# Performance work log

Hardware: AMD Instinct MI355X
Metric: run time of the kernel (lower is better)

## Reference

```python
import math
import jax, jax.numpy as jnp
import numpy as np

# h_data constants (init_kwargs)
PITCH = 0.0003      # [m]
FS = 40000000.0     # [Hz]
TX_ANGLE = 0.1      # [rad]
C = 1540.0          # [m/s]
T0 = 0.0            # [s]
CLIP = -70.0        # [dB]
EPS = np.float32(np.finfo(np.float32).eps)


def interplin(v, ds, sq):
    """Vectorized per-column linear interpolation: v(sq[:,k], k).
    v: (N, K) float, sq: (N, K) query points in physical units, ds: step size.
    """
    n = v.shape[0]
    iq = sq / ds
    oob = ~(iq < n - 2)
    iqc = jnp.where(oob, 0.0, iq)
    fl = jnp.floor(iqc).astype(jnp.int32)
    lw = iqc - fl
    v0 = jnp.take_along_axis(v, fl, axis=0)
    v1 = jnp.take_along_axis(v, fl + 1, axis=0)
    vq = v0 * (1.0 - lw) + v1 * lw
    return jnp.where(oob, 0.0, vq)


def fkmig(data):
    """Stolt f-k migration for one (nt, nx) plane-wave RF frame."""
    nt, nx = data.shape
    nt_shift = 2 * math.ceil(T0 * FS / 2)
    nt_fft = 4 * nt + nt_shift              # 8192
    nx_fft = 2 * math.ceil(4 * nx / 2)      # 512
    nf = nt_fft // 2 + 1                    # 4097

    f_vec = jnp.arange(nf, dtype=jnp.float32) * (FS / nt_fft)          # (nf,)
    kx_vec = jnp.roll(jnp.arange(-nx_fft // 2, nx_fft // 2, dtype=jnp.float32) + 1,
                      nx_fft // 2 + 1) / PITCH / nx_fft                # (nx_fft,)
    f = f_vec[:, None]    # (nf, 1)
    kx = kx_vec[None, :]  # (1, nx_fft)

    ol = jnp.fft.fft(data, nt_fft, axis=0)[:nf, :]                     # (nf, nx) complex

    sin_a = math.sin(TX_ANGLE)
    cos_a = math.cos(TX_ANGLE)
    t_delay = sin_a * ((nx - 1) * int(TX_ANGLE < 0)
                       - jnp.arange(nx, dtype=jnp.float32)) * (PITCH / C)  # (nx,)
    ol = ol * jnp.exp(-2j * math.pi * (t_delay + T0)[None, :] * f).astype(jnp.complex64)
    ol = jnp.fft.fft(ol, nx_fft, axis=1)                               # (nf, nx_fft)

    v_erm = C / math.sqrt(1 + cos_a + sin_a ** 2)
    beta = (1 + cos_a) ** 1.5 / (1 + cos_a + sin_a ** 2)
    kz = 2 * f / (beta * C)
    f_kz = v_erm * jnp.sqrt(kx ** 2 + kz ** 2)                         # (nf, nx_fft)

    evanescent = (jnp.abs(f) / (jnp.abs(kx) + EPS)) < C
    ol = jnp.where(evanescent, 0, ol)

    ds = FS / nt_fft
    ol = interplin(ol.real, ds, f_kz) + 1j * interplin(ol.imag, ds, f_kz)
    ol = ol * (f / (f_kz + EPS))
    ol = ol.at[0].set(0)

    # hermitian extension of the half spectrum
    oln = jnp.conj(jnp.fliplr(jnp.roll(ol, -1, axis=1)))
    inv_idx = jnp.arange(nt_fft // 2 - 1, 0, -1)
    ol = jnp.concatenate([ol, oln[inv_idx]], axis=0)                   # (nt_fft, nx_fft)
    ol = jnp.fft.ifft(ol, axis=0)

    gamma = sin_a / (2 - cos_a)
    dx = -gamma * (jnp.arange(nt_fft, dtype=jnp.float32) / FS) * C / 2
    ol = ol * jnp.exp(-2j * math.pi * kx_vec[None, :] * dx[:, None]).astype(jnp.complex64)
    ol = jnp.fft.ifft(ol, axis=1)
    return ol[nt_shift:nt_shift + nt, :nx]                             # (nt, nx) complex


def image_formation(mig):
    """Envelope detection (hilbert along axis 0) + log compression on (nt, nx) real."""
    nt = mig.shape[0]
    Xf = jnp.fft.fft(mig, nt, axis=0)
    h = np.zeros(nt, np.float32)
    if nt % 2 == 0:
        h[0] = h[nt // 2] = 1
        h[1:nt // 2] = 2
    else:
        h[0] = 1
        h[1:(nt + 1) // 2] = 2
    analytic = jnp.fft.ifft(Xf * jnp.asarray(h)[:, None], axis=0)
    img = 20.0 * jnp.log10(jnp.abs(analytic))
    img = img - jnp.max(img)
    img = jnp.where(img < CLIP, CLIP, img)
    return (img + abs(CLIP)) / abs(CLIP)


def setup_inputs() -> dict:
    key = jax.random.key(0)
    data = jax.random.normal(key, (4, 2048, 128), dtype=jnp.float32)
    return {"data": data}


def reference(data):
    mig = jax.vmap(fkmig)(data)                 # (B, nt, nx) complex
    img = jax.vmap(image_formation)(jnp.real(mig))
    return img
```

## Files before the change

kernel.cpp:

```cpp
#include <hip/hip_runtime.h>
#include <cmath>

#define NT 2048
#define NX 128
#define NXF 512
#define NF 4097
#define NFP 4104
#define TDP 2056
#define NBATCH 4
#define EPSF 1.1920929e-07f
#define SOUND_C 1540.0f

__device__ __forceinline__ int SK(int e) { return e + 2 * (e >> 4); }

struct FKP {
  float ds, inv_ds, inv_kx_den, v_erm, kz_coef, ph_rev, dx_coef;
};

__device__ __forceinline__ float2 cmul(float2 a, float2 b) {
  return make_float2(a.x * b.x - a.y * b.y, a.x * b.y + a.y * b.x);
}
__device__ __forceinline__ float2 twid(float u) {
  const float f = u - floorf(u);
  return make_float2(__builtin_amdgcn_cosf(f), __builtin_amdgcn_sinf(f));
}
__device__ __forceinline__ float2 twidf(float u) { return twid(u); }
__device__ __forceinline__ float2 twc16(int k, float sgn) {
  const float C[4]  = {1.0f, 0.923879532511f, 0.707106781187f, 0.382683432365f};
  const float Sn[4] = {0.0f, 0.382683432365f, 0.707106781187f, 0.923879532511f};
  return make_float2(C[k], sgn * Sn[k]);
}
__device__ __forceinline__ int dr4_3(unsigned m) {
  unsigned r = __brev(m) >> 26;
  return (int)(((r & 0x15u) << 1) | ((r >> 1) & 0x15u));
}
__device__ __forceinline__ int dr4_4(unsigned m) {
  unsigned r = __brev(m) >> 24;
  return (int)(((r & 0x55u) << 1) | ((r >> 1) & 0x55u));
}
__device__ __forceinline__ int dr4_5(unsigned m) {
  unsigned r = __brev(m) >> 22;
  return (int)(((r & 0x155u) << 1) | ((r >> 1) & 0x155u));
}

__device__ __forceinline__ void dft4(float2& A, float2& B, float2& C, float2& D, float sgn) {
  float2 t0 = make_float2(A.x + C.x, A.y + C.y);
  float2 t1 = make_float2(A.x - C.x, A.y - C.y);
  float2 t2 = make_float2(B.x + D.x, B.y + D.y);
  float2 t3 = make_float2(B.x - D.x, B.y - D.y);
  float2 r  = make_float2(-sgn * t3.y, sgn * t3.x);
  A = make_float2(t0.x + t2.x, t0.y + t2.y);
  B = make_float2(t1.x + r.x, t1.y + r.y);
  C = make_float2(t0.x - t2.x, t0.y - t2.y);
  D = make_float2(t1.x - r.x, t1.y - r.y);
}
__device__ __forceinline__ void bfly4r(float2& A, float2& B, float2& C, float2& D,
                                       float2 w1, float2 w2, float2 w3, float sgn) {
  B = cmul(B, w1); C = cmul(C, w2); D = cmul(D, w3);
  dft4(A, B, C, D, sgn);
}
__device__ __forceinline__ void twtrip(float u, float2& w1, float2& w2, float2& w3) {
  w1 = twid(u); w2 = cmul(w1, w1); w3 = cmul(w2, w1);
}

template<int S>
__device__ __forceinline__ void mstage(float2* __restrict__ s, int base, int kb, float sgn) {
  float2 w[16];
#pragma unroll
  for (int m = 0; m < 16; ++m) w[m] = s[SK(base + S * m)];
  {
    float2 a1, a2, a3; twtrip(sgn * (float)kb * (1.0f / (4 * S)), a1, a2, a3);
#pragma unroll
    for (int a = 0; a < 4; ++a)
      bfly4r(w[4 * a], w[4 * a + 1], w[4 * a + 2], w[4 * a + 3], a1, a2, a3, sgn);
  }
  {
    const float2 wb = twid(sgn * (float)kb * (1.0f / (16 * S)));
#pragma unroll
    for (int c = 0; c < 4; ++c) {
      float2 b1 = cmul(wb, twc16(c, sgn));
      float2 b2 = cmul(b1, b1);
      float2 b3 = cmul(b2, b1);
      bfly4r(w[c], w[4 + c], w[8 + c], w[12 + c], b1, b2, b3, sgn);
    }
  }
#pragma unroll
  for (int m = 0; m < 16; ++m) s[SK(base + S * m)] = w[m];
}

__global__ void __launch_bounds__(256) k_tr(const float* __restrict__ data,
                                            float* __restrict__ dt,
                                            float* __restrict__ red,
                                            size_t slot4, int b_base) {
  __shared__ float tile[32][33];
  if (threadIdx.x == 0 && blockIdx.x == 0 && blockIdx.y == 0)
    *(unsigned*)&red[blockIdx.z * slot4] = 0u;
  const int tx = threadIdx.x & 31;
  const int ty = threadIdx.x >> 5;
  const int t0 = blockIdx.x * 32;
  const int x0 = blockIdx.y * 32;
  const float* In = data + (size_t)(b_base + blockIdx.z) * NT * NX;
  float* Dt = dt + blockIdx.z * slot4;
  for (int i = ty; i < 32; i += 8)
    tile[i][tx] = In[(size_t)(t0 + i) * NX + x0 + tx];
  __syncthreads();
  for (int i = ty; i < 32; i += 8)
    Dt[(size_t)(x0 + i) * TDP + t0 + tx] = tile[tx][i];
}

__global__ void __launch_bounds__(256) k_fft_t(const float* __restrict__ dt,
                                               float2* __restrict__ o1t,
                                               size_t slot4, size_t slot8, FKP P) {
  __shared__ float2 nat[1152];
  __shared__ float2 s[4608];
  const int x = blockIdx.x, tid = threadIdx.x;
  const float2* row2 = (const float2*)(dt + blockIdx.z * slot4 + (size_t)x * TDP);
  float2* O1 = o1t + blockIdx.z * slot8 + (size_t)x * NFP;
  for (int m = tid; m < 1024; m += 256) nat[SK(m)] = row2[m];
  __syncthreads();
  {
    const int m0 = dr4_4((unsigned)tid);
    const float2 v0 = nat[SK(m0)];
    const float2 v1 = nat[SK(m0 + 256)];
    const float2 v2 = nat[SK(m0 + 512)];
    const float2 v3 = nat[SK(m0 + 768)];
    const int base = tid << 4;
#pragma unroll
    for (int k = 0; k < 4; ++k) {
      float2 A = v0, B = v1, C = v2, D = v3;
      if (k == 0) {
        dft4(A, B, C, D, -1.0f);
      } else {
        float2 w1 = twc16(k, -1.0f);
        float2 w2 = cmul(w1, w1);
        float2 w3 = cmul(w2, w1);
        bfly4r(A, B, C, D, w1, w2, w3, -1.0f);
      }
      s[SK(base + k)] = A; s[SK(base + 4 + k)] = B;
      s[SK(base + 8 + k)] = C; s[SK(base + 12 + k)] = D;
    }
  }
  __syncthreads();
  mstage<16>(s, ((tid >> 4) << 8) | (tid & 15), tid & 15, -1.0f);
  __syncthreads();
  mstage<256>(s, tid, tid, -1.0f);
  __syncthreads();
  for (int k = tid; k < NF; k += 256) {
    const int ka = k & 4095, kb = (4096 - k) & 4095;
    const float2 Ck = s[SK(ka)];
    const float2 Cm = s[SK(kb)];
    float2 E = make_float2(0.5f * (Ck.x + Cm.x), 0.5f * (Ck.y - Cm.y));
    float2 T = make_float2(0.5f * (Ck.x - Cm.x), 0.5f * (Ck.y + Cm.y));
    float2 WT = cmul(twid((float)k * (-1.0f / 8192.0f)), T);
    float2 X = make_float2(E.x + WT.y, E.y - WT.x);
    float2 ph = twidf(P.ph_rev * (float)(x * k));
    O1[k] = cmul(X, ph);
  }
}

#define R2P 580
__global__ void __launch_bounds__(512) k_fft_x(const float2* __restrict__ o1t,
                                               float2* __restrict__ ot,
                                               size_t slot8, FKP P) {
  __shared__ float2 s[8 * R2P];
  const int i0 = blockIdx.x * 8;
  const int tid = threadIdx.x;
  const float2* O1 = o1t + blockIdx.z * slot8;
  float2* OT = ot + blockIdx.z * slot8;
  for (int idx = tid; idx < 128 * 8; idx += 512) {
    const int ii = idx & 7, x = idx >> 3;
    const int i = i0 + ii;
    float2 v = (i < NF) ? O1[(size_t)x * NFP + i] : make_float2(0.f, 0.f);
    float2* r = s + ii * R2P;
    const int p = ((x & 1) << 8) + 4 * dr4_3((unsigned)(x >> 1));
    r[SK(p)] = v; r[SK(p + 1)] = v; r[SK(p + 2)] = v; r[SK(p + 3)] = v;
  }
  __syncthreads();
  for (int mh = 4; mh <= 64; mh *= 4) {
    const float inv = -1.0f / (float)(4 * mh);
    for (int t = tid; t < 8 * 128; t += 512) {
      const int row = t >> 7, tt = t & 127;
      const int half = tt >> 6, q = tt & 63;
      const int k = q & (mh - 1);
      const int i0b = ((q & ~(mh - 1)) << 2) + k + (half << 8);
      float2* r = s + row * R2P;
      float2 A = r[SK(i0b)], B = r[SK(i0b + mh)], C = r[SK(i0b + 2 * mh)], D = r[SK(i0b + 3 * mh)];
      float2 w1, w2, w3; twtrip((float)k * inv, w1, w2, w3);
      bfly4r(A, B, C, D, w1, w2, w3, -1.0f);
      r[SK(i0b)] = A; r[SK(i0b + mh)] = B; r[SK(i0b + 2 * mh)] = C; r[SK(i0b + 3 * mh)] = D;
    }
    __syncthreads();
  }
  for (int t = tid; t < 8 * 256; t += 512) {
    const int row = t >> 8, k = t & 255;
    float2* r = s + row * R2P;
    float2 E = r[SK(k)], O = r[SK(256 + k)];
    float2 WO = cmul(twid((float)k * (-1.0f / 512.0f)), O);
    r[SK(k)]       = make_float2(E.x + WO.x, E.y + WO.y);
    r[SK(256 + k)] = make_float2(E.x - WO.x, E.y - WO.y);
  }
  __syncthreads();
  for (int idx = tid; idx < 512 * 8; idx += 512) {
    const int j = idx >> 3, ii = idx & 7;
    const int i = i0 + ii;
    if (i >= NF) continue;
    const float f = P.ds * (float)i;
    const int kn = (j <= 256) ? j : j - 512;
    const float kx = fabsf((float)kn * P.inv_kx_den);
    float2 v = (f / (kx + EPSF) < SOUND_C) ? make_float2(0.f, 0.f)
                                           : s[ii * R2P + SK(j)];
    OT[(size_t)j * NFP + i] = v;
  }
}

__global__ void __launch_bounds__(512) k_ifft_t(const float2* __restrict__ ot,
                                                float2* __restrict__ tdt,
                                                size_t slot8, FKP P) {
  __shared__ float2 s[9216];
  const int j = blockIdx.x;
  const int jm = (NXF - j) & (NXF - 1);
  const int t = threadIdx.x;
  const float2* OT = ot + blockIdx.z * slot8;
  float2* T = tdt + blockIdx.z * slot8 + (size_t)j * TDP;
  const float kxj = (float)j * P.inv_kx_den;
  const float kx2 = kxj * kxj;
  const float2* rowj = OT + (size_t)j * NFP;
  const float2* rowm = OT + (size_t)jm * NFP;
  {
    const int tau = t & 255, half = t >> 8;
    const int m0 = dr4_4((unsigned)tau);
    float2 w[16];
#pragma unroll
    for (int m = 0; m < 16; ++m) {
      const int ci = (m & 3) * 1024 + (m >> 2) * 256 + m0;
      const int n = 2 * ci + half;
      const bool mir = (n > 4096);
      const int r = mir ? (8192 - n) : n;
      const float2* rw = mir ? rowm : rowj;
      float2 v = make_float2(0.f, 0.f);
      if (r > 0) {
        const float f = P.ds * (float)r;
        const float kz = f * P.kz_coef;
        const float fkz = P.v_erm * sqrtf(kx2 + kz * kz);
        const float iq = fkz * P.inv_ds;
        if (iq < 4095.0f) {
          const float flf = floorf(iq);
          const int fl = (int)flf;
          const float lw = iq - flf;
          const float2 v0 = rw[fl], v1 = rw[fl + 1];
          const float sc = f / (fkz + EPSF);
          v.x = (v0.x + (v1.x - v0.x) * lw) * sc;
          v.y = (v0.y + (v1.y - v0.y) * lw) * (mir ? -sc : sc);
        }
      }
      w[m] = v;
    }
#pragma unroll
    for (int a = 0; a < 4; ++a) dft4(w[4 * a], w[4 * a + 1], w[4 * a + 2], w[4 * a + 3], 1.0f);
    dft4(w[0], w[4], w[8], w[12], 1.0f);
#pragma unroll
    for (int k = 1; k < 4; ++k) {
      float2 w1 = twc16(k, 1.0f);
      float2 w2 = cmul(w1, w1);
      float2 w3 = cmul(w2, w1);
      bfly4r(w[k], w[4 + k], w[8 + k], w[12 + k], w1, w2, w3, 1.0f);
    }
    const int base = t << 4;
#pragma unroll
    for (int m = 0; m < 16; ++m) s[SK(base + m)] = w[m];
  }
  __syncthreads();
  mstage<16>(s, ((t >> 4) << 8) | (t & 15), t & 15, 1.0f);
  __syncthreads();
  mstage<256>(s, ((t >> 8) << 12) | (t & 255), t & 255, 1.0f);
  __syncthreads();
  const float dxr = -kxj * P.dx_coef;
#pragma unroll
  for (int i = 0; i < 4; ++i) {
    const int k = t + 512 * i;
    const float2 E = s[SK(k)];
    const float2 O = s[SK(4096 + k)];
    const float2 WO = cmul(twid((float)k * (1.0f / 8192.0f)), O);
    const float2 y = make_float2(E.x + WO.x, E.y + WO.y);
    T[k] = cmul(y, twidf(dxr * (float)k));
  }
}

#define SXA 260
#define SXC 292
__global__ void __launch_bounds__(256) k_c2r_x(const float2* __restrict__ tdt,
                                               float* __restrict__ migt,
                                               size_t slot8, size_t slot4) {
  __shared__ float2 sx[8 * SXA];
  __shared__ float2 sc[8 * SXC];
  const int t0 = blockIdx.x * 8;
  const int tid = threadIdx.x;
  const float2* T = tdt + blockIdx.z * slot8;
  float* M = migt + blockIdx.z * slot4;
  for (int idx = tid; idx < 257 * 8; idx += 256) {
    const int tt = idx & 7, jj = idx >> 3;
    float2 v = T[(size_t)jj * TDP + t0 + tt];
    if (jj == 0 || jj == 256) v.y = 0.0f;
    sx[tt * SXA + jj] = v;
  }
  __syncthreads();
  for (int idx = tid; idx < 129 * 8; idx += 256) {
    const int row = idx & 7, k = idx >> 3;
    const float2* X = sx + row * SXA;
    float2* Cb = sc + row * SXC;
    const float2 Xk = X[k];
    const float2 Xm = X[256 - k];
    float2 Ef = make_float2(0.5f * (Xk.x + Xm.x), 0.5f * (Xk.y - Xm.y));
    float2 Tm = make_float2(0.5f * (Xk.x - Xm.x), 0.5f * (Xk.y + Xm.y));
    float2 Of = cmul(twid((float)k * (1.0f / 512.0f)), Tm);
    Cb[SK(dr4_4((unsigned)k))] = make_float2(Ef.x - Of.y, Ef.y + Of.x);
    if (k > 0 && k < 128)
      Cb[SK(dr4_4((unsigned)(256 - k)))] = make_float2(Ef.x + Of.y, Of.x - Ef.y);
  }
  __syncthreads();
  for (int mh = 1; mh <= 64; mh *= 4) {
    const float inv = 1.0f / (float)(4 * mh);
    for (int t = tid; t < 8 * 64; t += 256) {
      const int row = t >> 6, q = t & 63;
      const int k = q & (mh - 1);
      const int i0 = ((q & ~(mh - 1)) << 2) + k;
      float2* r = sc + row * SXC;
      float2 A = r[SK(i0)], B = r[SK(i0 + mh)], C = r[SK(i0 + 2 * mh)], D = r[SK(i0 + 3 * mh)];
      if (mh > 1) {
        float2 w1, w2, w3; twtrip((float)k * inv, w1, w2, w3);
        bfly4r(A, B, C, D, w1, w2, w3, 1.0f);
      } else {
        dft4(A, B, C, D, 1.0f);
      }
      r[SK(i0)] = A; r[SK(i0 + mh)] = B; r[SK(i0 + 2 * mh)] = C; r[SK(i0 + 3 * mh)] = D;
    }
    __syncthreads();
  }
  for (int idx = tid; idx < 128 * 8; idx += 256) {
    const int x = idx >> 3, tt = idx & 7;
    const float2 c = sc[tt * SXC + SK(x >> 1)];
    M[(size_t)x * TDP + t0 + tt] = (x & 1) ? c.y : c.x;
  }
}

__global__ void __launch_bounds__(512) k_hilbert(const float* __restrict__ migt,
                                                 float* __restrict__ migdb,
                                                 float* __restrict__ red,
                                                 size_t slot4) {
  __shared__ float2 s[2304];
  __shared__ float rmax[512];
  const int x = blockIdx.x, tid = threadIdx.x;
  const float* Mr = migt + blockIdx.z * slot4 + (size_t)x * TDP;
  float* Db = migdb + blockIdx.z * slot4 + (size_t)x * TDP;
#pragma unroll
  for (int i = 0; i < 4; ++i) {
    const int p = tid + 512 * i;
    s[SK(p)] = make_float2(Mr[p], 0.0f);
  }
  __syncthreads();
#pragma unroll
  for (int i = 0; i < 2; ++i) {
    const int p = tid + 512 * i;
    const float2 a = s[SK(p)], b = s[SK(p + 1024)];
    s[SK(p)] = make_float2(a.x + b.x, a.y + b.y);
    s[SK(p + 1024)] = cmul(make_float2(a.x - b.x, a.y - b.y),
                           twid(-(float)p * (1.0f / 2048.0f)));
  }
  __syncthreads();
  for (int mh = 256; mh >= 1; mh >>= 2) {
    const int half = tid >> 8, q = tid & 255;
    const int k = q & (mh - 1);
    const int i0 = (half << 10) + ((q & ~(mh - 1)) << 2) + k;
    float2 A = s[SK(i0)], B = s[SK(i0 + mh)], C = s[SK(i0 + 2 * mh)], D = s[SK(i0 + 3 * mh)];
    dft4(A, B, C, D, -1.0f);
    if (mh > 1) {
      float2 w1, w2, w3; twtrip(-(float)k / (float)(4 * mh), w1, w2, w3);
      B = cmul(B, w1); C = cmul(C, w2); D = cmul(D, w3);
    }
    s[SK(i0)] = A; s[SK(i0 + mh)] = B; s[SK(i0 + 2 * mh)] = C; s[SK(i0 + 3 * mh)] = D;
    __syncthreads();
  }
#pragma unroll
  for (int i = 0; i < 4; ++i) {
    const int p = tid + 512 * i;
    const int kk = 2 * dr4_5((unsigned)(p & 1023)) + (p >> 10);
    const float hv = (kk == 0 || kk == 1024) ? 1.0f : ((kk < 1024) ? 2.0f : 0.0f);
    float2 v = s[SK(p)];
    s[SK(p)] = make_float2(v.x * hv, v.y * hv);
  }
  __syncthreads();
  for (int mh = 1; mh <= 256; mh <<= 2) {
    const int half = tid >> 8, q = tid & 255;
    const int k = q & (mh - 1);
    const int i0 = (half << 10) + ((q & ~(mh - 1)) << 2) + k;
    float2 A = s[SK(i0)], B = s[SK(i0 + mh)], C = s[SK(i0 + 2 * mh)], D = s[SK(i0 + 3 * mh)];
    if (mh > 1) {
      float2 w1, w2, w3; twtrip((float)k / (float)(4 * mh), w1, w2, w3);
      bfly4r(A, B, C, D, w1, w2, w3, 1.0f);
    } else {
      dft4(A, B, C, D, 1.0f);
    }
    s[SK(i0)] = A; s[SK(i0 + mh)] = B; s[SK(i0 + 2 * mh)] = C; s[SK(i0 + 3 * mh)] = D;
    __syncthreads();
  }
  float lmax = -3.0e38f;
#pragma unroll
  for (int i = 0; i < 2; ++i) {
    const int p = tid + 512 * i;
    const float2 E = s[SK(p)];
    const float2 O = cmul(s[SK(p + 1024)], twid((float)p * (1.0f / 2048.0f)));
    const float2 y0 = make_float2(E.x + O.x, E.y + O.y);
    const float2 y1 = make_float2(E.x - O.x, E.y - O.y);
    const float d0 = 10.0f * __log10f(fmaxf(y0.x * y0.x + y0.y * y0.y, 1e-30f));
    const float d1 = 10.0f * __log10f(fmaxf(y1.x * y1.x + y1.y * y1.y, 1e-30f));
    Db[p] = d0; Db[p + 1024] = d1;
    lmax = fmaxf(lmax, fmaxf(d0, d1));
  }
  rmax[tid] = lmax;
  __syncthreads();
  for (int w = 256; w > 0; w >>= 1) {
    if (tid < w) rmax[tid] = fmaxf(rmax[tid], rmax[tid + w]);
    __syncthreads();
  }
  if (tid == 0) {
    const unsigned sb = __float_as_uint(rmax[0]);
    const unsigned key = (sb & 0x80000000u) ? ~sb : (sb | 0x80000000u);
    atomicMax((unsigned*)&red[blockIdx.z * slot4], key);
  }
}

__global__ void __launch_bounds__(256) k_norm_tr(const float* __restrict__ migdb,
                                                 const float* __restrict__ red,
                                                 float* __restrict__ out,
                                                 size_t slot4, int b_base) {
  __shared__ float tile[32][33];
  const int tx = threadIdx.x & 31;
  const int ty = threadIdx.x >> 5;
  const int t0 = blockIdx.x * 32;
  const int x0 = blockIdx.y * 32;
  const float* Db = migdb + blockIdx.z * slot4;
  const unsigned kk = *(const unsigned*)&red[blockIdx.z * slot4];
  const float mx = (kk & 0x80000000u) ? __uint_as_float(kk & 0x7FFFFFFFu)
                                      : __uint_as_float(~kk);
  float* O = out + (size_t)(b_base + blockIdx.z) * NT * NX;
  for (int i = ty; i < 32; i += 8)
    tile[i][tx] = Db[(size_t)(x0 + i) * TDP + t0 + tx];
  __syncthreads();
  for (int i = ty; i < 32; i += 8) {
    float v = tile[tx][i] - mx;
    v = fmaxf(v, -70.0f);
    O[(size_t)(t0 + i) * NX + x0 + tx] = (v + 70.0f) * (1.0f / 70.0f);
  }
}

extern "C" void kernel_launch(void* const* d_in, const int* in_sizes, int n_in,
                              void* d_out, int out_size, void* d_ws, size_t ws_size,
                              hipStream_t stream) {
  const float* data = (const float*)d_in[0];
  float* out = (float*)d_out;
  char* ws = (char*)d_ws;

  const size_t O1T_B = 0;
  const size_t OT_B  = (size_t)NX * NFP * sizeof(float2);
  const size_t TDT_B = OT_B + (size_t)NXF * NFP * sizeof(float2);
  const size_t RED_B = TDT_B + (size_t)257 * TDP * sizeof(float2);
  const size_t SLOT_B = ((RED_B + 1024 + 4095) / 4096) * 4096;
  const size_t slot4 = SLOT_B / 4, slot8 = SLOT_B / 8;
  const int slots = (ws_size >= (size_t)NBATCH * SLOT_B) ? NBATCH : 1;

  FKP P;
  {
    const double SA = std::sin(0.1), CA = std::cos(0.1);
    const double A1 = 1.0 + CA + SA * SA;
    const double beta = std::pow(1.0 + CA, 1.5) / A1;
    const double ds = 40000000.0 / 8192.0;
    P.ds = (float)ds;
    P.inv_ds = (float)(8192.0 / 40000000.0);
    P.inv_kx_den = (float)(1.0 / (0.0003 * 512.0));
    P.v_erm = (float)(1540.0 / std::sqrt(A1));
    P.kz_coef = (float)(2.0 / (beta * 1540.0));
    P.ph_rev = (float)(SA * 0.0003 * ds / 1540.0);
    P.dx_coef = (float)(-(SA / (2.0 - CA)) * 1540.0 / (2.0 * 40000000.0));
  }

  float2* o1t  = (float2*)(ws + O1T_B);
  float*  migt = (float*)(ws + O1T_B);
  float2* ot   = (float2*)(ws + OT_B);
  float2* tdt  = (float2*)(ws + TDT_B);
  float*  scr4 = (float*)(ws + TDT_B);
  float*  red  = (float*)(ws + RED_B);

  for (int b0 = 0; b0 < NBATCH; b0 += slots) {
    k_tr     <<<dim3(64, 4, slots), 256, 0, stream>>>(data, scr4, red, slot4, b0);
    k_fft_t  <<<dim3(NX, 1, slots), 256, 0, stream>>>(scr4, o1t, slot4, slot8, P);
    k_fft_x  <<<dim3(513, 1, slots), 512, 0, stream>>>(o1t, ot, slot8, P);
    k_ifft_t <<<dim3(257, 1, slots), 512, 0, stream>>>(ot, tdt, slot8, P);
    k_c2r_x  <<<dim3(256, 1, slots), 256, 0, stream>>>(tdt, migt, slot8, slot4);
    k_hilbert<<<dim3(NX, 1, slots), 512, 0, stream>>>(migt, scr4, red, slot4);
    k_norm_tr<<<dim3(64, 4, slots), 256, 0, stream>>>(scr4, red, out, slot4, b0);
  }
}
```

Before: 156.8 us.

## Restructure x-FFT kernel to register-resident first stages with fused final butterfly

Rewrites the k_fft_x kernel so each of 256 threads loads four inputs into registers and performs the first two radix-4 stages there, instead of writing replicated zero-padded values to shared memory and running separate butterfly passes. The last radix-2 stage is fused into the output loop, which computes both halves on the fly while applying the evanescent mask. This cuts shared-memory traffic and the number of barriers. It also halves the block size. The trade-off is more redundant twiddle and butterfly work in the output loop and fewer threads per block.

```diff
diff --git a/kernel.cpp b/kernel.cpp
--- a/kernel.cpp
+++ b/kernel.cpp
@@ -159,7 +159,7 @@
 }
 
 #define R2P 580
-__global__ void __launch_bounds__(512) k_fft_x(const float2* __restrict__ o1t,
+__global__ void __launch_bounds__(256) k_fft_x(const float2* __restrict__ o1t,
                                                float2* __restrict__ ot,
                                                size_t slot8, FKP P) {
   __shared__ float2 s[8 * R2P];
@@ -167,49 +167,53 @@
   const int tid = threadIdx.x;
   const float2* O1 = o1t + blockIdx.z * slot8;
   float2* OT = ot + blockIdx.z * slot8;
-  for (int idx = tid; idx < 128 * 8; idx += 512) {
-    const int ii = idx & 7, x = idx >> 3;
-    const int i = i0 + ii;
-    float2 v = (i < NF) ? O1[(size_t)x * NFP + i] : make_float2(0.f, 0.f);
-    float2* r = s + ii * R2P;
-    const int p = ((x & 1) << 8) + 4 * dr4_3((unsigned)(x >> 1));
-    r[SK(p)] = v; r[SK(p + 1)] = v; r[SK(p + 2)] = v; r[SK(p + 3)] = v;
-  }
-  __syncthreads();
-  for (int mh = 4; mh <= 64; mh *= 4) {
-    const float inv = -1.0f / (float)(4 * mh);
-    for (int t = tid; t < 8 * 128; t += 512) {
-      const int row = t >> 7, tt = t & 127;
-      const int half = tt >> 6, q = tt & 63;
-      const int k = q & (mh - 1);
-      const int i0b = ((q & ~(mh - 1)) << 2) + k + (half << 8);
-      float2* r = s + row * R2P;
-      float2 A = r[SK(i0b)], B = r[SK(i0b + mh)], C = r[SK(i0b + 2 * mh)], D = r[SK(i0b + 3 * mh)];
-      float2 w1, w2, w3; twtrip((float)k * inv, w1, w2, w3);
-      bfly4r(A, B, C, D, w1, w2, w3, -1.0f);
-      r[SK(i0b)] = A; r[SK(i0b + mh)] = B; r[SK(i0b + 2 * mh)] = C; r[SK(i0b + 3 * mh)] = D;
-    }
-    __syncthreads();
-  }
-  for (int t = tid; t < 8 * 256; t += 512) {
-    const int row = t >> 8, k = t & 255;
+  const int row = tid & 7, hu = tid >> 3;
+  const int b = hu & 1, u = hu >> 1;
+  const int i = i0 + row;
+  {
+    float2 v[4];
+#pragma unroll
+    for (int c = 0; c < 4; ++c) {
+      const int m = dr4_3((unsigned)(4 * u + c));
+      const int xx = 2 * m + b;
+      v[c] = (i < NF) ? O1[(size_t)xx * NFP + i] : make_float2(0.f, 0.f);
+    }
     float2* r = s + row * R2P;
-    float2 E = r[SK(k)], O = r[SK(256 + k)];
-    float2 WO = cmul(twid((float)k * (-1.0f / 512.0f)), O);
-    r[SK(k)]       = make_float2(E.x + WO.x, E.y + WO.y);
-    r[SK(256 + k)] = make_float2(E.x - WO.x, E.y - WO.y);
-  }
-  __syncthreads();
-  for (int idx = tid; idx < 512 * 8; idx += 512) {
+    const int base = (b << 8) + (u << 4);
+#pragma unroll
+    for (int k = 0; k < 4; ++k) {
+      float2 A = v[0], B = v[1], C = v[2], D = v[3];
+      if (k == 0) {
+        dft4(A, B, C, D, -1.0f);
+      } else {
+        float2 w1 = twc16(k, -1.0f);
+        float2 w2 = cmul(w1, w1);
+        float2 w3 = cmul(w2, w1);
+        bfly4r(A, B, C, D, w1, w2, w3, -1.0f);
+      }
+      r[SK(base + k)] = A; r[SK(base + 4 + k)] = B;
+      r[SK(base + 8 + k)] = C; r[SK(base + 12 + k)] = D;
+    }
+  }
+  __syncthreads();
+  mstage<16>(s + row * R2P, (b << 8) + u, u, -1.0f);
+  __syncthreads();
+  for (int idx = tid; idx < 512 * 8; idx += 256) {
     const int j = idx >> 3, ii = idx & 7;
-    const int i = i0 + ii;
-    if (i >= NF) continue;
-    const float f = P.ds * (float)i;
+    const int io = i0 + ii;
+    if (io >= NF) continue;
+    const int k = j & 255;
+    const float2* r = s + ii * R2P;
+    const float2 E = r[SK(k)];
+    const float2 O = r[SK(256 + k)];
+    const float2 WO = cmul(twid((float)k * (-1.0f / 512.0f)), O);
+    float2 vv = (j < 256) ? make_float2(E.x + WO.x, E.y + WO.y)
+                          : make_float2(E.x - WO.x, E.y - WO.y);
+    const float f = P.ds * (float)io;
     const int kn = (j <= 256) ? j : j - 512;
     const float kx = fabsf((float)kn * P.inv_kx_den);
-    float2 v = (f / (kx + EPSF) < SOUND_C) ? make_float2(0.f, 0.f)
-                                           : s[ii * R2P + SK(j)];
-    OT[(size_t)j * NFP + i] = v;
+    if (f / (kx + EPSF) < SOUND_C) vv = make_float2(0.f, 0.f);
+    OT[(size_t)j * NFP + io] = vv;
   }
 }
 
@@ -493,7 +497,7 @@
   for (int b0 = 0; b0 < NBATCH; b0 += slots) {
     k_tr     <<<dim3(64, 4, slots), 256, 0, stream>>>(data, scr4, red, slot4, b0);
     k_fft_t  <<<dim3(NX, 1, slots), 256, 0, stream>>>(scr4, o1t, slot4, slot8, P);
-    k_fft_x  <<<dim3(513, 1, slots), 512, 0, stream>>>(o1t, ot, slot8, P);
+    k_fft_x  <<<dim3(513, 1, slots), 256, 0, stream>>>(o1t, ot, slot8, P);
     k_ifft_t <<<dim3(257, 1, slots), 512, 0, stream>>>(ot, tdt, slot8, P);
     k_c2r_x  <<<dim3(256, 1, slots), 256, 0, stream>>>(tdt, migt, slot8, slot4);
     k_hilbert<<<dim3(NX, 1, slots), 512, 0, stream>>>(migt, scr4, red, slot4);
```

New measurement: 161.4 us. +2.9%, slower.
